# Performance work log

Hardware: AMD Instinct MI355X
Metric: run time of the kernel (lower is better)

## Reference

```python
import jax, jax.numpy as jnp
import numpy as np

STRIDE = (1, 1)
PADDING = ((1, 1), (1, 1))


def setup_inputs() -> dict:
    key = jax.random.key(0)
    k1, k2 = jax.random.split(key)
    x = jax.random.normal(k1, (32, 256, 56, 56), dtype=jnp.float32)
    # kaiming-uniform-like init scale (matches _ConvNd.reset_parameters magnitude roughly)
    fan_in = 256 * 3 * 3
    bound = float(np.sqrt(1.0 / fan_in))
    weight = jax.random.uniform(k2, (256, 256, 3, 3), dtype=jnp.float32,
                                minval=-bound, maxval=bound)
    return {"x": x, "weight": weight}


def reference(x, weight):
    # per-output-filter mean of |w| over (in_ch, kh, kw)
    a = jnp.mean(jnp.abs(weight), axis=(1, 2, 3), keepdims=True)  # [O,1,1,1]
    b = jnp.sign(weight)
    binary_weight = b * a
    out = jax.lax.conv_general_dilated(
        x, binary_weight,
        window_strides=STRIDE,
        padding=PADDING,
        dimension_numbers=("NCHW", "OIHW", "NCHW"),
    )
    return out
```

## Files before the change

### kernel.cpp

```cpp
#include <hip/hip_runtime.h>
#include <cstdint>
#include <cstddef>

#define XP_BYTES 55115776ull
#define WB_OFF   55115776ull
#define AL_OFF   (WB_OFF + 1179648ull)

typedef __bf16 bf16x8 __attribute__((ext_vector_type(8)));
typedef float  f32x4  __attribute__((ext_vector_type(4)));

static __device__ __forceinline__ unsigned short f2bf(float f) {
  union { float f; unsigned int u; } v; v.f = f;
  unsigned int u = v.u;
  u += 0x7FFFu + ((u >> 16) & 1u);
  return (unsigned short)(u >> 16);
}

static __device__ __forceinline__ void async16(void* lds, const void* g) {
  __builtin_amdgcn_global_load_lds(
      (const __attribute__((address_space(1))) unsigned int*)g,
      (__attribute__((address_space(3))) unsigned int*)lds, 16, 0, 0);
}

__global__ void prep_w(const float* __restrict__ w, unsigned short* __restrict__ wb,
                       float* __restrict__ alpha) {
  const int o = blockIdx.x, c = threadIdx.x;
  const float* wr = w + (size_t)(o * 256 + c) * 9;
  float s = 0.f;
#pragma unroll
  for (int tap = 0; tap < 9; ++tap) {
    float v = wr[tap];
    s += fabsf(v);
    unsigned short sg = (v > 0.f) ? 0x3F80u : ((v < 0.f) ? 0xBF80u : 0u);
    wb[(size_t)o * 2304 + tap * 256 + c] = sg;
  }
  __shared__ float red[256];
  red[c] = s;
  __syncthreads();
  for (int d = 128; d > 0; d >>= 1) {
    if (c < d) red[c] += red[c + d];
    __syncthreads();
  }
  if (c == 0) alpha[o] = red[0] * (1.f / 2304.f);
}

__global__ void prep_x(const float* __restrict__ x, unsigned short* __restrict__ xp) {
  const int bx = blockIdx.x;
  const int n = bx / 58, hp = bx % 58;
  const int t = threadIdx.x;
  unsigned short* row = xp + (size_t)(n * 58 + hp) * 58 * 256;

  if (hp == 0 || hp == 57) {
    uint32_t* r32 = (uint32_t*)row;
    for (int i = t; i < 7424; i += 256) r32[i] = 0;
    return;
  }
  const int h = hp - 1;
  const int c2 = (t & 127) * 2;
  const int rep = t >> 7;
  const int w0 = rep * 28;
  const float* x0 = x + ((size_t)(n * 256 + c2) * 56 + h) * 56;
  const float* x1 = x0 + (size_t)56 * 56;

  if (rep == 0) {
    ((uint32_t*)row)[c2 >> 1] = 0;
    ((uint32_t*)(row + 57 * 256))[c2 >> 1] = 0;
  }
#pragma unroll
  for (int i = 0; i < 7; ++i) {
    float4 a = *(const float4*)(x0 + w0 + i * 4);
    float4 b = *(const float4*)(x1 + w0 + i * 4);
    unsigned short va[4] = {f2bf(a.x), f2bf(a.y), f2bf(a.z), f2bf(a.w)};
    unsigned short vb[4] = {f2bf(b.x), f2bf(b.y), f2bf(b.z), f2bf(b.w)};
    const int wbase = w0 + i * 4;
#pragma unroll
    for (int j = 0; j < 4; ++j) {
      uint32_t pack = (uint32_t)va[j] | ((uint32_t)vb[j] << 16);
      ((uint32_t*)(row + (size_t)(wbase + j + 1) * 256))[c2 >> 1] = pack;
    }
  }
}

__global__ __launch_bounds__(256, 3)
void conv_mfma(const unsigned short* __restrict__ xp,
               const unsigned short* __restrict__ wb,
               const float* __restrict__ alpha,
               float* __restrict__ out) {
  __shared__ __align__(16) char lds[16384];
  char* ldsA = lds;
  char* ldsB = lds + 8192;

  const int tid = threadIdx.x;
  const int wave = tid >> 6, lane = tid & 63;
  const int wm = wave >> 1, wn = wave & 1;
  const int o0 = (blockIdx.x & 1) * 128;
  const int pix0 = (blockIdx.x >> 1) * 128;

  const int chunk = lane & 3;
  const int rsub = lane >> 2;

  const char* wbB = (const char*)wb;
  const char* xpB = (const char*)xp;
  const char* gA[2];
  const char* gB[2];
#pragma unroll
  for (int j = 0; j < 2; ++j) {
    const int row = (wave * 2 + j) * 16 + rsub;
    gA[j] = wbB + ((size_t)(o0 + row) * 2304 + chunk * 8) * 2;
    const int pix = pix0 + row;
    const int n = pix / 3136, rem = pix % 3136;
    const int h = rem / 56, w = rem % 56;
    gB[j] = xpB + (size_t)((n * 58 + h) * 58 + w) * 512 + chunk * 16;
  }

  f32x4 acc[4][4];
#pragma unroll
  for (int i = 0; i < 4; ++i)
#pragma unroll
    for (int j = 0; j < 4; ++j) acc[i][j] = (f32x4){0.f, 0.f, 0.f, 0.f};

  const int ar = lane & 15, aq = lane >> 4;

  for (int tap = 0; tap < 9; ++tap) {
    const int kh = tap / 3, kw = tap % 3;
    const int tapoff = (kh * 58 + kw) * 512;
#pragma unroll
    for (int cc = 0; cc < 8; ++cc) {
      const int kA = (tap * 256 + cc * 32) * 2;
      const int kB = tapoff + cc * 64;
      __syncthreads();
      async16(ldsA + (wave * 2 + 0) * 1024, gA[0] + kA);
      async16(ldsA + (wave * 2 + 1) * 1024, gA[1] + kA);
      async16(ldsB + (wave * 2 + 0) * 1024, gB[0] + kB);
      async16(ldsB + (wave * 2 + 1) * 1024, gB[1] + kB);
      __syncthreads();

      bf16x8 af[4], bfr[4];
#pragma unroll
      for (int mi = 0; mi < 4; ++mi)
        af[mi] = *(const bf16x8*)(ldsA + ((wm * 64 + mi * 16 + ar) * 64 + aq * 16));
#pragma unroll
      for (int ni = 0; ni < 4; ++ni)
        bfr[ni] = *(const bf16x8*)(ldsB + ((wn * 64 + ni * 16 + ar) * 64 + aq * 16));
#pragma unroll
      for (int mi = 0; mi < 4; ++mi)
#pragma unroll
        for (int ni = 0; ni < 4; ++ni)
          acc[mi][ni] = __builtin_amdgcn_mfma_f32_16x16x32_bf16(af[mi], bfr[ni], acc[mi][ni], 0, 0, 0);
    }
  }

  int nc[4], rc[4];
#pragma unroll
  for (int ni = 0; ni < 4; ++ni) {
    const int pix = pix0 + wn * 64 + ni * 16 + ar;
    nc[ni] = pix / 3136; rc[ni] = pix % 3136;
  }
#pragma unroll
  for (int mi = 0; mi < 4; ++mi) {
    const int orow = o0 + wm * 64 + mi * 16 + aq * 4;
    float al[4];
#pragma unroll
    for (int r = 0; r < 4; ++r) al[r] = alpha[orow + r];
#pragma unroll
    for (int ni = 0; ni < 4; ++ni) {
      const size_t base = (size_t)nc[ni] * 802816 + (size_t)orow * 3136 + (size_t)rc[ni];
#pragma unroll
      for (int r = 0; r < 4; ++r)
        out[base + (size_t)r * 3136] = acc[mi][ni][r] * al[r];
    }
  }
}

extern "C" void kernel_launch(void* const* d_in, const int* in_sizes, int n_in,
                              void* d_out, int out_size, void* d_ws, size_t ws_size,
                              hipStream_t stream) {
  const float* x = (const float*)d_in[0];
  const float* w = (const float*)d_in[1];
  char* ws = (char*)d_ws;
  unsigned short* xp  = (unsigned short*)ws;
  unsigned short* wbp = (unsigned short*)(ws + WB_OFF);
  float* alpha = (float*)(ws + AL_OFF);
  float* out = (float*)d_out;

  prep_w<<<256, 256, 0, stream>>>(w, wbp, alpha);
  prep_x<<<32 * 58, 256, 0, stream>>>(x, xp);
  conv_mfma<<<1568, 256, 0, stream>>>(xp, wbp, alpha, out);
}
```

Measured before the change: 350.2 us.

## Double-buffer conv LDS stages and transpose input prep through shared memory

The conv main loop moves from two barriers per K-step to a ping-pong LDS buffer. The next step's global-to-LDS async loads are issued before the MFMA work on the current buffer, so load latency can overlap compute. LDS grows to 32 KB and the occupancy hint drops from 3 to 2 blocks per CU. The input NCHW-to-padded-NHWC bf16 conversion now goes through a swizzled LDS tile so global writes are 16-byte coalesced, and halo zeroing moves to its own small kernel.

After: 346.8 us. Within noise of the previous version (-1.0%).

```diff
diff --git a/kernel.cpp b/kernel.cpp
--- a/kernel.cpp
+++ b/kernel.cpp
@@ -8,6 +8,7 @@
 
 typedef __bf16 bf16x8 __attribute__((ext_vector_type(8)));
 typedef float  f32x4  __attribute__((ext_vector_type(4)));
+typedef unsigned short u16x8 __attribute__((ext_vector_type(8)));
 
 static __device__ __forceinline__ unsigned short f2bf(float f) {
   union { float f; unsigned int u; } v; v.f = f;
@@ -44,51 +45,62 @@
   if (c == 0) alpha[o] = red[0] * (1.f / 2304.f);
 }
 
+__global__ void zero_halo(unsigned short* __restrict__ xp) {
+  const int n = blockIdx.x;
+  const int t = threadIdx.x;
+  uint32_t* base = (uint32_t*)(xp + (size_t)n * 58 * 58 * 256);
+  uint32_t* r57 = base + 57 * 7424;
+  for (int i = t; i < 7424; i += 1024) { base[i] = 0; r57[i] = 0; }
+  for (int i = t; i < 7168; i += 1024) {
+    const int r = i >> 7, c = i & 127;
+    base[(size_t)((r + 1) * 58) * 128 + c] = 0;
+    base[(size_t)((r + 1) * 58 + 57) * 128 + c] = 0;
+  }
+}
+
 __global__ void prep_x(const float* __restrict__ x, unsigned short* __restrict__ xp) {
+  __shared__ unsigned short tile[64 * 256];
   const int bx = blockIdx.x;
-  const int n = bx / 58, hp = bx % 58;
-  const int t = threadIdx.x;
-  unsigned short* row = xp + (size_t)(n * 58 + hp) * 58 * 256;
-
-  if (hp == 0 || hp == 57) {
-    uint32_t* r32 = (uint32_t*)row;
-    for (int i = t; i < 7424; i += 256) r32[i] = 0;
-    return;
-  }
-  const int h = hp - 1;
-  const int c2 = (t & 127) * 2;
-  const int rep = t >> 7;
-  const int w0 = rep * 28;
-  const float* x0 = x + ((size_t)(n * 256 + c2) * 56 + h) * 56;
-  const float* x1 = x0 + (size_t)56 * 56;
-
-  if (rep == 0) {
-    ((uint32_t*)row)[c2 >> 1] = 0;
-    ((uint32_t*)(row + 57 * 256))[c2 >> 1] = 0;
-  }
-#pragma unroll
-  for (int i = 0; i < 7; ++i) {
-    float4 a = *(const float4*)(x0 + w0 + i * 4);
-    float4 b = *(const float4*)(x1 + w0 + i * 4);
-    unsigned short va[4] = {f2bf(a.x), f2bf(a.y), f2bf(a.z), f2bf(a.w)};
-    unsigned short vb[4] = {f2bf(b.x), f2bf(b.y), f2bf(b.z), f2bf(b.w)};
-    const int wbase = w0 + i * 4;
+  const int n = bx / 49, pt = bx % 49;
+  const int p0 = pt * 64;
+  const int tid = threadIdx.x;
+  const int f = tid & 15;
+  const int cg = tid >> 4;
+  const float* xn = x + (size_t)n * 256 * 3136 + p0 + f * 4;
+
+#pragma unroll
+  for (int i = 0; i < 16; ++i) {
+    const int c = cg + i * 16;
+    const float4 v = *(const float4*)(xn + (size_t)c * 3136);
+    unsigned short b[4] = {f2bf(v.x), f2bf(v.y), f2bf(v.z), f2bf(v.w)};
 #pragma unroll
     for (int j = 0; j < 4; ++j) {
-      uint32_t pack = (uint32_t)va[j] | ((uint32_t)vb[j] << 16);
-      ((uint32_t*)(row + (size_t)(wbase + j + 1) * 256))[c2 >> 1] = pack;
+      const int pix = f * 4 + j;
+      const int cs = c ^ (((pix >> 2) & 3) << 3) ^ (((pix >> 4) & 3) << 5);
+      tile[pix * 256 + cs] = b[j];
     }
   }
-}
-
-__global__ __launch_bounds__(256, 3)
+  __syncthreads();
+
+  const int c8 = (tid & 31) * 8;
+  const int psub = tid >> 5;
+#pragma unroll
+  for (int pass = 0; pass < 8; ++pass) {
+    const int pl = psub + pass * 8;
+    const int p = p0 + pl;
+    const int h = p / 56, w = p % 56;
+    const int cs = c8 ^ (((pl >> 2) & 3) << 3) ^ (((pl >> 4) & 3) << 5);
+    const u16x8 v = *(const u16x8*)&tile[pl * 256 + cs];
+    *(u16x8*)(xp + ((size_t)(n * 58 + h + 1) * 58 + (w + 1)) * 256 + c8) = v;
+  }
+}
+
+__global__ __launch_bounds__(256, 2)
 void conv_mfma(const unsigned short* __restrict__ xp,
                const unsigned short* __restrict__ wb,
                const float* __restrict__ alpha,
                float* __restrict__ out) {
-  __shared__ __align__(16) char lds[16384];
-  char* ldsA = lds;
-  char* ldsB = lds + 8192;
+  __shared__ __align__(16) char lds[32768];
 
   const int tid = threadIdx.x;
   const int wave = tid >> 6, lane = tid & 63;
@@ -121,33 +133,40 @@
 
   const int ar = lane & 15, aq = lane >> 4;
 
-  for (int tap = 0; tap < 9; ++tap) {
-    const int kh = tap / 3, kw = tap % 3;
-    const int tapoff = (kh * 58 + kw) * 512;
-#pragma unroll
-    for (int cc = 0; cc < 8; ++cc) {
-      const int kA = (tap * 256 + cc * 32) * 2;
-      const int kB = tapoff + cc * 64;
-      __syncthreads();
-      async16(ldsA + (wave * 2 + 0) * 1024, gA[0] + kA);
-      async16(ldsA + (wave * 2 + 1) * 1024, gA[1] + kA);
-      async16(ldsB + (wave * 2 + 0) * 1024, gB[0] + kB);
-      async16(ldsB + (wave * 2 + 1) * 1024, gB[1] + kB);
-      __syncthreads();
-
-      bf16x8 af[4], bfr[4];
-#pragma unroll
-      for (int mi = 0; mi < 4; ++mi)
-        af[mi] = *(const bf16x8*)(ldsA + ((wm * 64 + mi * 16 + ar) * 64 + aq * 16));
+  auto stage = [&](int b, int ks) {
+    const int tap = ks >> 3;
+    const int tapoff = ((tap / 3) * 58 + (tap % 3)) * 512;
+    const int kA = ks * 64;
+    const int kB = tapoff + (ks & 7) * 64;
+    char* LA = lds + b * 16384;
+    char* LB = LA + 8192;
+    async16(LA + (wave * 2 + 0) * 1024, gA[0] + kA);
+    async16(LA + (wave * 2 + 1) * 1024, gA[1] + kA);
+    async16(LB + (wave * 2 + 0) * 1024, gB[0] + kB);
+    async16(LB + (wave * 2 + 1) * 1024, gB[1] + kB);
+  };
+
+  stage(0, 0);
+#pragma unroll 2
+  for (int ks = 0; ks < 72; ++ks) {
+    const int cur = ks & 1;
+    __syncthreads();
+    if (ks < 71) stage(cur ^ 1, ks + 1);
+
+    const char* LA = lds + cur * 16384;
+    const char* LB = LA + 8192;
+    bf16x8 af[4], bfr[4];
+#pragma unroll
+    for (int mi = 0; mi < 4; ++mi)
+      af[mi] = *(const bf16x8*)(LA + ((wm * 64 + mi * 16 + ar) * 64 + aq * 16));
+#pragma unroll
+    for (int ni = 0; ni < 4; ++ni)
+      bfr[ni] = *(const bf16x8*)(LB + ((wn * 64 + ni * 16 + ar) * 64 + aq * 16));
+#pragma unroll
+    for (int mi = 0; mi < 4; ++mi)
 #pragma unroll
       for (int ni = 0; ni < 4; ++ni)
-        bfr[ni] = *(const bf16x8*)(ldsB + ((wn * 64 + ni * 16 + ar) * 64 + aq * 16));
-#pragma unroll
-      for (int mi = 0; mi < 4; ++mi)
-#pragma unroll
-        for (int ni = 0; ni < 4; ++ni)
-          acc[mi][ni] = __builtin_amdgcn_mfma_f32_16x16x32_bf16(af[mi], bfr[ni], acc[mi][ni], 0, 0, 0);
-    }
+        acc[mi][ni] = __builtin_amdgcn_mfma_f32_16x16x32_bf16(af[mi], bfr[ni], acc[mi][ni], 0, 0, 0);
   }
 
   int nc[4], rc[4];
@@ -183,7 +202,8 @@
   float* alpha = (float*)(ws + AL_OFF);
   float* out = (float*)d_out;
 
+  zero_halo<<<32, 1024, 0, stream>>>(xp);
   prep_w<<<256, 256, 0, stream>>>(w, wbp, alpha);
-  prep_x<<<32 * 58, 256, 0, stream>>>(x, xp);
+  prep_x<<<32 * 49, 256, 0, stream>>>(x, xp);
   conv_mfma<<<1568, 256, 0, stream>>>(xp, wbp, alpha, out);
 }
```
